# Kernel tuning notes

Hardware: AMD Instinct MI355X
Metric: run time of the kernel (lower is better)

## Reference

```python
import jax, jax.numpy as jnp
import numpy as np

N_NODES = 100000
N_EDGES = 3200000
N_FEAT = 128
HIDDEN = 16
N_CLASSES = 10
N_GRAPHS = 512


def setup_inputs() -> dict:
    key = jax.random.key(0)
    ks = jax.random.split(key, 12)
    x = jax.random.normal(ks[0], (N_NODES, N_FEAT), dtype=jnp.float32)
    edge_index = jax.random.randint(ks[1], (2, N_EDGES), 0, N_NODES, dtype=jnp.int64)
    batch = jnp.sort(jax.random.randint(ks[2], (N_NODES,), 0, N_GRAPHS, dtype=jnp.int64))
    def glorot(k, fan_in, fan_out):
        s = jnp.sqrt(6.0 / (fan_in + fan_out)).astype(jnp.float32)
        return jax.random.uniform(k, (fan_in, fan_out), jnp.float32, -s, s)
    W1 = glorot(ks[3], N_FEAT, HIDDEN); b1 = jnp.zeros((HIDDEN,), jnp.float32)
    W2 = glorot(ks[4], HIDDEN, HIDDEN); b2 = jnp.zeros((HIDDEN,), jnp.float32)
    W3 = glorot(ks[5], HIDDEN, HIDDEN); b3 = jnp.zeros((HIDDEN,), jnp.float32)
    Wlin = glorot(ks[6], HIDDEN, N_CLASSES)
    blin = jnp.zeros((N_CLASSES,), jnp.float32)
    return {"x": x, "edge_index": edge_index, "batch": batch,
            "W1": W1, "b1": b1, "W2": W2, "b2": b2, "W3": W3, "b3": b3,
            "Wlin": Wlin, "blin": blin}


def _gcn_conv(x, W, b, src, dst, norm, n):
    # h = X W ; out[dst] += norm * h[src] ; + bias
    h = x @ W
    out = jax.ops.segment_sum(h[src] * norm[:, None], dst, num_segments=n)
    return out + b


def reference(x, edge_index, batch, W1, b1, W2, b2, W3, b3, Wlin, blin):
    n = x.shape[0]
    loop = jnp.arange(n, dtype=edge_index.dtype)
    src = jnp.concatenate([edge_index[0], loop])  # add self-loops (PyG GCNConv default)
    dst = jnp.concatenate([edge_index[1], loop])
    # symmetric degree normalization: deg over destination (incl. self-loops)
    deg = jax.ops.segment_sum(jnp.ones_like(dst, dtype=x.dtype), dst, num_segments=n)
    dinv = jnp.where(deg > 0, jax.lax.rsqrt(jnp.maximum(deg, 1.0)), 0.0)
    norm = dinv[src] * dinv[dst]  # [E+N]

    h = jax.nn.relu(_gcn_conv(x, W1, b1, src, dst, norm, n))
    h = jax.nn.relu(_gcn_conv(h, W2, b2, src, dst, norm, n))
    h = _gcn_conv(h, W3, b3, src, dst, norm, n)
    # global add pool over graphs
    pooled = jax.ops.segment_sum(h, batch, num_segments=N_GRAPHS)  # [G, hidden]
    # dropout p=0.5 is identity in eval mode
    return pooled @ Wlin + blin
```

## Files before the change

kernel.cpp:

```cpp
#include <hip/hip_runtime.h>
#include <hip/hip_fp16.h>

#define N_NODES   100000
#define N_EDGES   3200000
#define N_FEAT    128
#define HIDDEN    16
#define N_CLASSES 10
#define N_GRAPHS  512
#define NPB       256
#define NBUCKET   391
#define EPB       8192
#define PBLK      ((N_EDGES + EPB - 1) / EPB)
#define PSLACK    12288
#define CSLACK    9216


__global__ void cursor_init_kernel(int* __restrict__ cur) {
    int i = blockIdx.x * 256 + threadIdx.x;
    if (i < NBUCKET) cur[i] = i * PSLACK;
}

__global__ __launch_bounds__(512) void partition_kernel(const int* __restrict__ src,
                                                        const int* __restrict__ dst,
                                                        int* __restrict__ cur,
                                                        unsigned* __restrict__ part) {
    __shared__ int cnt[NBUCKET];
    __shared__ int lbase[NBUCKET];
    __shared__ int rk[NBUCKET];
    __shared__ int gbase[NBUCKET];
    __shared__ int s[512];
    __shared__ unsigned sorted[EPB];
    int tid = threadIdx.x;
    for (int i = tid; i < NBUCKET; i += 512) cnt[i] = 0;
    __syncthreads();
    int s0 = blockIdx.x * EPB;
#pragma unroll
    for (int i = 0; i < EPB / 512; ++i) {
        int e = s0 + i * 512 + tid;
        if (e < N_EDGES) atomicAdd(&cnt[dst[e] >> 8], 1);
    }
    __syncthreads();
    int v = (tid < NBUCKET) ? cnt[tid] : 0;
    s[tid] = v;
    __syncthreads();
    for (int off = 1; off < 512; off <<= 1) {
        int t = (tid >= off) ? s[tid - off] : 0;
        __syncthreads();
        s[tid] += t;
        __syncthreads();
    }
    if (tid < NBUCKET) {
        int lb = s[tid] - v;
        lbase[tid] = lb;
        rk[tid]    = lb;
        int cpad = (v + 15) & ~15;
        gbase[tid] = cpad ? atomicAdd(&cur[tid], cpad) : 0;
    }
    __syncthreads();
#pragma unroll
    for (int i = 0; i < EPB / 512; ++i) {
        int e = s0 + i * 512 + tid;
        if (e < N_EDGES) {
            int d = dst[e];
            int b = d >> 8;
            int r = atomicAdd(&rk[b], 1);
            sorted[r] = (unsigned)src[e] | ((unsigned)(d & 255) << 17);
        }
    }
    __syncthreads();
    int wave = tid >> 6, lane = tid & 63;
    for (int b = wave; b < NBUCKET; b += 8) {
        int c = cnt[b];
        if (!c) continue;
        int cpad = (c + 15) & ~15;
        int lb = lbase[b], gb = gbase[b];
        for (int j = lane; j < cpad; j += 64)
            part[gb + j] = (j < c) ? sorted[lb + j] : 0xFFFFFFFFu;
    }
}

__global__ void build_csr_kernel(const unsigned* __restrict__ part, const int* __restrict__ cur,
                                 int* __restrict__ rp_beg, int* __restrict__ rp_end,
                                 float* __restrict__ dinv, int* __restrict__ csr) {
    __shared__ int ncnt[256];
    __shared__ int s[256];
    int b   = blockIdx.x;
    int tid = threadIdx.x;
    int beg = b * PSLACK, end = cur[b];
    ncnt[tid] = 0;
    __syncthreads();
    for (int j = beg + tid; j < end; j += 256) {
        unsigned r = part[j];
        if (r != 0xFFFFFFFFu) atomicAdd(&ncnt[(r >> 17) & 255], 1);
    }
    __syncthreads();
    int deg = ncnt[tid];
    s[tid] = deg;
    __syncthreads();
    for (int off = 1; off < 256; off <<= 1) {
        int t = (tid >= off) ? s[tid - off] : 0;
        __syncthreads();
        s[tid] += t;
        __syncthreads();
    }
    int excl = s[tid] - deg;
    int node = b * 256 + tid;
    int cbeg = b * CSLACK;
    if (node < N_NODES) {
        rp_beg[node] = cbeg + excl;
        rp_end[node] = cbeg + excl + deg;
        dinv[node]   = rsqrtf((float)(deg + 1));
    }
    ncnt[tid] = cbeg + excl;
    __syncthreads();
    for (int j = beg + tid; j < end; j += 256) {
        unsigned r = part[j];
        if (r != 0xFFFFFFFFu) {
            int v = (r >> 17) & 255;
            int slot = atomicAdd(&ncnt[v], 1);
            csr[slot] = (int)(r & 0x1FFFFu);
        }
    }
}


__device__ __forceinline__ void pack_store_row(__half* dstp, int v, const float* o) {
    int4 w0, w1;
    __half2 q;
    q = __floats2half2_rn(o[0],  o[1]);  w0.x = *(int*)&q;
    q = __floats2half2_rn(o[2],  o[3]);  w0.y = *(int*)&q;
    q = __floats2half2_rn(o[4],  o[5]);  w0.z = *(int*)&q;
    q = __floats2half2_rn(o[6],  o[7]);  w0.w = *(int*)&q;
    q = __floats2half2_rn(o[8],  o[9]);  w1.x = *(int*)&q;
    q = __floats2half2_rn(o[10], o[11]); w1.y = *(int*)&q;
    q = __floats2half2_rn(o[12], o[13]); w1.z = *(int*)&q;
    q = __floats2half2_rn(o[14], o[15]); w1.w = *(int*)&q;
    ((int4*)dstp)[v * 2]     = w0;
    ((int4*)dstp)[v * 2 + 1] = w1;
}

__global__ void transform_x_kernel(const float* __restrict__ x, const float* __restrict__ W,
                                   const float* __restrict__ dinv, __half* __restrict__ g) {
    __shared__ float Wl[N_FEAT * HIDDEN];
    int tid = threadIdx.x;
    for (int i = tid; i < N_FEAT * HIDDEN; i += 256) Wl[i] = W[i];
    __syncthreads();
    int v = blockIdx.x * 256 + tid;
    if (v >= N_NODES) return;
    float acc[HIDDEN];
#pragma unroll
    for (int f = 0; f < HIDDEN; ++f) acc[f] = 0.f;
    const float4* xr = (const float4*)(x + (size_t)v * N_FEAT);
#pragma unroll 4
    for (int k4 = 0; k4 < N_FEAT / 4; ++k4) {
        float4 xv = xr[k4];
        const float* wr = &Wl[k4 * 4 * HIDDEN];
#pragma unroll
        for (int f = 0; f < HIDDEN; ++f)
            acc[f] += xv.x * wr[f] + xv.y * wr[HIDDEN + f] +
                      xv.z * wr[2 * HIDDEN + f] + xv.w * wr[3 * HIDDEN + f];
    }
    float di = dinv[v];
#pragma unroll
    for (int f = 0; f < HIDDEN; ++f) acc[f] *= di;
    pack_store_row(g, v, acc);
}

__global__ void transform_h_kernel(const __half* __restrict__ h, const float* __restrict__ W,
                                   const float* __restrict__ dinv, __half* __restrict__ g) {
    __shared__ float Wl[HIDDEN * HIDDEN];
    int tid = threadIdx.x;
    if (tid < HIDDEN * HIDDEN) Wl[tid] = W[tid];
    __syncthreads();
    int v = blockIdx.x * 256 + tid;
    if (v >= N_NODES) return;
    int4 r0 = ((const int4*)h)[v * 2];
    int4 r1 = ((const int4*)h)[v * 2 + 1];
    float hv[HIDDEN];
    {
        const int rr[8] = {r0.x, r0.y, r0.z, r0.w, r1.x, r1.y, r1.z, r1.w};
#pragma unroll
        for (int q = 0; q < 8; ++q) {
            __half2 p = *(const __half2*)&rr[q];
            float2 f2 = __half22float2(p);
            hv[q * 2] = f2.x; hv[q * 2 + 1] = f2.y;
        }
    }
    float acc[HIDDEN];
#pragma unroll
    for (int f = 0; f < HIDDEN; ++f) acc[f] = 0.f;
#pragma unroll
    for (int k = 0; k < HIDDEN; ++k) {
        float hk = hv[k];
#pragma unroll
        for (int f = 0; f < HIDDEN; ++f) acc[f] += hk * Wl[k * HIDDEN + f];
    }
    float di = dinv[v];
#pragma unroll
    for (int f = 0; f < HIDDEN; ++f) acc[f] *= di;
    pack_store_row(g, v, acc);
}

__global__ void aggregate_kernel(const __half* __restrict__ g, const int* __restrict__ rp_beg,
                                 const int* __restrict__ rp_end, const int* __restrict__ csr,
                                 const float* __restrict__ dinv, const float* __restrict__ bias,
                                 __half* __restrict__ hout, int do_relu) {
    int tid  = threadIdx.x;
    int wave = tid >> 6;
    int l    = tid & 63;
    int c  = l >> 3;
    int vl = (l >> 1) & 3;
    int hh = l & 1;
    int v = blockIdx.x * 16 + wave * 4 + vl;
    if (v >= N_NODES) return;
    int beg = rp_beg[v];
    int deg = rp_end[v] - beg;
    int j0 = beg + ((deg * c) >> 3);
    int j1 = beg + ((deg * (c + 1)) >> 3);
    const int4* g4 = (const int4*)g;
    float a0 = 0.f, a1 = 0.f, a2 = 0.f, a3 = 0.f, a4 = 0.f, a5 = 0.f, a6 = 0.f, a7 = 0.f;
#pragma unroll 4
    for (int j = j0; j < j1; ++j) {
        int s = csr[j];
        int4 r = g4[s * 2 + hh];
        float2 f0 = __half22float2(*(const __half2*)&r.x);
        float2 f1 = __half22float2(*(const __half2*)&r.y);
        float2 f2 = __half22float2(*(const __half2*)&r.z);
        float2 f3 = __half22float2(*(const __half2*)&r.w);
        a0 += f0.x; a1 += f0.y; a2 += f1.x; a3 += f1.y;
        a4 += f2.x; a5 += f2.y; a6 += f3.x; a7 += f3.y;
    }
    a0 += __shfl_xor(a0, 8);  a1 += __shfl_xor(a1, 8);
    a2 += __shfl_xor(a2, 8);  a3 += __shfl_xor(a3, 8);
    a4 += __shfl_xor(a4, 8);  a5 += __shfl_xor(a5, 8);
    a6 += __shfl_xor(a6, 8);  a7 += __shfl_xor(a7, 8);
    a0 += __shfl_xor(a0, 16); a1 += __shfl_xor(a1, 16);
    a2 += __shfl_xor(a2, 16); a3 += __shfl_xor(a3, 16);
    a4 += __shfl_xor(a4, 16); a5 += __shfl_xor(a5, 16);
    a6 += __shfl_xor(a6, 16); a7 += __shfl_xor(a7, 16);
    a0 += __shfl_xor(a0, 32); a1 += __shfl_xor(a1, 32);
    a2 += __shfl_xor(a2, 32); a3 += __shfl_xor(a3, 32);
    a4 += __shfl_xor(a4, 32); a5 += __shfl_xor(a5, 32);
    a6 += __shfl_xor(a6, 32); a7 += __shfl_xor(a7, 32);
    if (c == 0) {
        int4 r = g4[v * 2 + hh];
        float2 s0 = __half22float2(*(const __half2*)&r.x);
        float2 s1 = __half22float2(*(const __half2*)&r.y);
        float2 s2 = __half22float2(*(const __half2*)&r.z);
        float2 s3 = __half22float2(*(const __half2*)&r.w);
        float di = dinv[v];
        const float4* bp = (const float4*)bias;
        float4 bA = bp[hh * 2];
        float4 bB = bp[hh * 2 + 1];
        float o0 = di * (a0 + s0.x) + bA.x;
        float o1 = di * (a1 + s0.y) + bA.y;
        float o2 = di * (a2 + s1.x) + bA.z;
        float o3 = di * (a3 + s1.y) + bA.w;
        float o4 = di * (a4 + s2.x) + bB.x;
        float o5 = di * (a5 + s2.y) + bB.y;
        float o6 = di * (a6 + s3.x) + bB.z;
        float o7 = di * (a7 + s3.y) + bB.w;
        if (do_relu) {
            o0 = fmaxf(o0, 0.f); o1 = fmaxf(o1, 0.f); o2 = fmaxf(o2, 0.f); o3 = fmaxf(o3, 0.f);
            o4 = fmaxf(o4, 0.f); o5 = fmaxf(o5, 0.f); o6 = fmaxf(o6, 0.f); o7 = fmaxf(o7, 0.f);
        }
        int4 w;
        __half2 q;
        q = __floats2half2_rn(o0, o1); w.x = *(int*)&q;
        q = __floats2half2_rn(o2, o3); w.y = *(int*)&q;
        q = __floats2half2_rn(o4, o5); w.z = *(int*)&q;
        q = __floats2half2_rn(o6, o7); w.w = *(int*)&q;
        ((int4*)hout)[v * 2 + hh] = w;
    }
}


__global__ void pool_head_kernel(const __half* __restrict__ h, const int* __restrict__ batch,
                                 const float* __restrict__ Wlin, const float* __restrict__ blin,
                                 float* __restrict__ out) {
    __shared__ float red[256];
    __shared__ int bounds[2];
    int g   = blockIdx.x;
    int tid = threadIdx.x;
    if (tid < 2) {
        int target = g + tid;
        int lo = 0, hi = N_NODES;
        while (lo < hi) {
            int mid = (lo + hi) >> 1;
            if (batch[mid] < target) lo = mid + 1; else hi = mid;
        }
        bounds[tid] = lo;
    }
    __syncthreads();
    int start = bounds[0], end = bounds[1];
    int f = tid & 15, r = tid >> 4;
    float acc = 0.f;
    for (int v = start + r; v < end; v += 16)
        acc += __half2float(h[v * HIDDEN + f]);
    red[tid] = acc;
    __syncthreads();
    for (int off = 128; off >= 16; off >>= 1) {
        if (tid < off) red[tid] += red[tid + off];
        __syncthreads();
    }
    if (tid < N_CLASSES) {
        float s = blin[tid];
#pragma unroll
        for (int fe = 0; fe < HIDDEN; ++fe) s += red[fe] * Wlin[fe * N_CLASSES + tid];
        out[g * N_CLASSES + tid] = s;
    }
}


extern "C" void kernel_launch(void* const* d_in, const int* in_sizes, int n_in,
                              void* d_out, int out_size, void* d_ws, size_t ws_size,
                              hipStream_t stream) {
    const float* x     = (const float*)d_in[0];
    const int*   ei    = (const int*)d_in[1];
    const int*   src   = ei;
    const int*   dst   = ei + N_EDGES;
    const int*   batch = (const int*)d_in[2];
    const float* W1 = (const float*)d_in[3];
    const float* b1 = (const float*)d_in[4];
    const float* W2 = (const float*)d_in[5];
    const float* b2 = (const float*)d_in[6];
    const float* W3 = (const float*)d_in[7];
    const float* b3 = (const float*)d_in[8];
    const float* Wlin = (const float*)d_in[9];
    const float* blin = (const float*)d_in[10];
    float* out = (float*)d_out;

    char* w = (char*)d_ws;
    auto alloc = [&](size_t bytes) -> char* {
        char* p = w;
        w += (bytes + 255) & ~(size_t)255;
        return p;
    };
    int*    cur    = (int*)alloc((size_t)NBUCKET * 4);
    int*    rp_beg = (int*)alloc((size_t)N_NODES * 4);
    int*    rp_end = (int*)alloc((size_t)N_NODES * 4);
    float*  dinv   = (float*)alloc((size_t)N_NODES * 4);
    __half* g      = (__half*)alloc((size_t)N_NODES * HIDDEN * 2);
    __half* hA     = (__half*)alloc((size_t)N_NODES * HIDDEN * 2);
    __half* hB     = (__half*)alloc((size_t)N_NODES * HIDDEN * 2);
    unsigned* part = (unsigned*)alloc((size_t)NBUCKET * PSLACK * 4);
    int*    csr    = (int*)alloc((size_t)NBUCKET * CSLACK * 4);

    int nbn = (N_NODES + 255) / 256;
    int ab  = (N_NODES + 15) / 16;

    cursor_init_kernel<<<(NBUCKET + 255) / 256, 256, 0, stream>>>(cur);
    partition_kernel<<<PBLK, 512, 0, stream>>>(src, dst, cur, part);
    build_csr_kernel<<<NBUCKET, 256, 0, stream>>>(part, cur, rp_beg, rp_end, dinv, csr);

    transform_x_kernel<<<nbn, 256, 0, stream>>>(x, W1, dinv, g);
    aggregate_kernel<<<ab, 256, 0, stream>>>(g, rp_beg, rp_end, csr, dinv, b1, hA, 1);
    transform_h_kernel<<<nbn, 256, 0, stream>>>(hA, W2, dinv, g);
    aggregate_kernel<<<ab, 256, 0, stream>>>(g, rp_beg, rp_end, csr, dinv, b2, hB, 1);
    transform_h_kernel<<<nbn, 256, 0, stream>>>(hB, W3, dinv, g);
    aggregate_kernel<<<ab, 256, 0, stream>>>(g, rp_beg, rp_end, csr, dinv, b3, hA, 0);

    pool_head_kernel<<<N_GRAPHS, 256, 0, stream>>>(hA, batch, Wlin, blin, out);
}
```

Baseline: 289.2 us.

## Fuse next-layer transform into aggregation, stage CSR in LDS, retune partition/CSR build

The next layer's 16x16 transform and dinv scaling move into the aggregate epilogue, which removes the two transform_h launches and their round trip of the hidden features through memory. Each aggregate block now covers 64 nodes and stages that range of CSR indices in shared memory when it fits. The partition kernel uses half as many edges per block with larger bucket slack and 16-lane store groups, and build_csr runs with 512 threads. Per-block work rises, and degree-skewed blocks can overflow the LDS buffer and fall back to global reads.

```diff
diff --git a/kernel.cpp b/kernel.cpp
--- a/kernel.cpp
+++ b/kernel.cpp
@@ -9,10 +9,11 @@
 #define N_GRAPHS  512
 #define NPB       256
 #define NBUCKET   391
-#define EPB       8192
+#define EPB       4096
 #define PBLK      ((N_EDGES + EPB - 1) / EPB)
-#define PSLACK    12288
+#define PSLACK    15872
 #define CSLACK    9216
+#define LDSE      3200
 
 
 __global__ void cursor_init_kernel(int* __restrict__ cur) {
@@ -68,75 +69,74 @@
         }
     }
     __syncthreads();
-    int wave = tid >> 6, lane = tid & 63;
-    for (int b = wave; b < NBUCKET; b += 8) {
+    int w16 = tid >> 4, l16 = tid & 15;
+    for (int b = w16; b < NBUCKET; b += 32) {
         int c = cnt[b];
         if (!c) continue;
         int cpad = (c + 15) & ~15;
         int lb = lbase[b], gb = gbase[b];
-        for (int j = lane; j < cpad; j += 64)
+        for (int j = l16; j < cpad; j += 16)
             part[gb + j] = (j < c) ? sorted[lb + j] : 0xFFFFFFFFu;
     }
 }
 
-__global__ void build_csr_kernel(const unsigned* __restrict__ part, const int* __restrict__ cur,
-                                 int* __restrict__ rp_beg, int* __restrict__ rp_end,
-                                 float* __restrict__ dinv, int* __restrict__ csr) {
+__global__ __launch_bounds__(512) void build_csr_kernel(const unsigned* __restrict__ part,
+                                                        const int* __restrict__ cur,
+                                                        int* __restrict__ rp_beg, int* __restrict__ rp_end,
+                                                        float* __restrict__ dinv, int* __restrict__ csr) {
     __shared__ int ncnt[256];
-    __shared__ int s[256];
+    __shared__ int s[512];
     int b   = blockIdx.x;
     int tid = threadIdx.x;
     int beg = b * PSLACK, end = cur[b];
-    ncnt[tid] = 0;
-    __syncthreads();
-    for (int j = beg + tid; j < end; j += 256) {
+    if (tid < 256) ncnt[tid] = 0;
+    __syncthreads();
+    for (int j = beg + tid; j < end; j += 512) {
         unsigned r = part[j];
         if (r != 0xFFFFFFFFu) atomicAdd(&ncnt[(r >> 17) & 255], 1);
     }
     __syncthreads();
-    int deg = ncnt[tid];
+    int deg = (tid < 256) ? ncnt[tid] : 0;
     s[tid] = deg;
     __syncthreads();
-    for (int off = 1; off < 256; off <<= 1) {
+    for (int off = 1; off < 512; off <<= 1) {
         int t = (tid >= off) ? s[tid - off] : 0;
         __syncthreads();
         s[tid] += t;
         __syncthreads();
     }
     int excl = s[tid] - deg;
-    int node = b * 256 + tid;
     int cbeg = b * CSLACK;
-    if (node < N_NODES) {
-        rp_beg[node] = cbeg + excl;
-        rp_end[node] = cbeg + excl + deg;
-        dinv[node]   = rsqrtf((float)(deg + 1));
-    }
-    ncnt[tid] = cbeg + excl;
-    __syncthreads();
-    for (int j = beg + tid; j < end; j += 256) {
+    if (tid < 256) {
+        int node = b * 256 + tid;
+        if (node < N_NODES) {
+            rp_beg[node] = cbeg + excl;
+            rp_end[node] = cbeg + excl + deg;
+            dinv[node]   = rsqrtf((float)(deg + 1));
+        }
+    }
+    __syncthreads();
+    if (tid < 256) ncnt[tid] = cbeg + excl;
+    __syncthreads();
+    for (int j = beg + tid; j < end; j += 512) {
         unsigned r = part[j];
         if (r != 0xFFFFFFFFu) {
-            int v = (r >> 17) & 255;
-            int slot = atomicAdd(&ncnt[v], 1);
+            int vv = (r >> 17) & 255;
+            int slot = atomicAdd(&ncnt[vv], 1);
             csr[slot] = (int)(r & 0x1FFFFu);
         }
     }
 }
 
 
-__device__ __forceinline__ void pack_store_row(__half* dstp, int v, const float* o) {
-    int4 w0, w1;
+__device__ __forceinline__ void pack_store8(__half* outp, int idx, const float* o) {
+    int4 w;
     __half2 q;
-    q = __floats2half2_rn(o[0],  o[1]);  w0.x = *(int*)&q;
-    q = __floats2half2_rn(o[2],  o[3]);  w0.y = *(int*)&q;
-    q = __floats2half2_rn(o[4],  o[5]);  w0.z = *(int*)&q;
-    q = __floats2half2_rn(o[6],  o[7]);  w0.w = *(int*)&q;
-    q = __floats2half2_rn(o[8],  o[9]);  w1.x = *(int*)&q;
-    q = __floats2half2_rn(o[10], o[11]); w1.y = *(int*)&q;
-    q = __floats2half2_rn(o[12], o[13]); w1.z = *(int*)&q;
-    q = __floats2half2_rn(o[14], o[15]); w1.w = *(int*)&q;
-    ((int4*)dstp)[v * 2]     = w0;
-    ((int4*)dstp)[v * 2 + 1] = w1;
+    q = __floats2half2_rn(o[0], o[1]); w.x = *(int*)&q;
+    q = __floats2half2_rn(o[2], o[3]); w.y = *(int*)&q;
+    q = __floats2half2_rn(o[4], o[5]); w.z = *(int*)&q;
+    q = __floats2half2_rn(o[6], o[7]); w.w = *(int*)&q;
+    ((int4*)outp)[idx] = w;
 }
 
 __global__ void transform_x_kernel(const float* __restrict__ x, const float* __restrict__ W,
@@ -163,114 +163,122 @@
     float di = dinv[v];
 #pragma unroll
     for (int f = 0; f < HIDDEN; ++f) acc[f] *= di;
-    pack_store_row(g, v, acc);
-}
-
-__global__ void transform_h_kernel(const __half* __restrict__ h, const float* __restrict__ W,
-                                   const float* __restrict__ dinv, __half* __restrict__ g) {
-    __shared__ float Wl[HIDDEN * HIDDEN];
-    int tid = threadIdx.x;
-    if (tid < HIDDEN * HIDDEN) Wl[tid] = W[tid];
-    __syncthreads();
-    int v = blockIdx.x * 256 + tid;
-    if (v >= N_NODES) return;
-    int4 r0 = ((const int4*)h)[v * 2];
-    int4 r1 = ((const int4*)h)[v * 2 + 1];
-    float hv[HIDDEN];
-    {
-        const int rr[8] = {r0.x, r0.y, r0.z, r0.w, r1.x, r1.y, r1.z, r1.w};
-#pragma unroll
-        for (int q = 0; q < 8; ++q) {
-            __half2 p = *(const __half2*)&rr[q];
-            float2 f2 = __half22float2(p);
-            hv[q * 2] = f2.x; hv[q * 2 + 1] = f2.y;
-        }
-    }
-    float acc[HIDDEN];
-#pragma unroll
-    for (int f = 0; f < HIDDEN; ++f) acc[f] = 0.f;
-#pragma unroll
-    for (int k = 0; k < HIDDEN; ++k) {
-        float hk = hv[k];
-#pragma unroll
-        for (int f = 0; f < HIDDEN; ++f) acc[f] += hk * Wl[k * HIDDEN + f];
-    }
-    float di = dinv[v];
-#pragma unroll
-    for (int f = 0; f < HIDDEN; ++f) acc[f] *= di;
-    pack_store_row(g, v, acc);
-}
-
-__global__ void aggregate_kernel(const __half* __restrict__ g, const int* __restrict__ rp_beg,
-                                 const int* __restrict__ rp_end, const int* __restrict__ csr,
-                                 const float* __restrict__ dinv, const float* __restrict__ bias,
-                                 __half* __restrict__ hout, int do_relu) {
-    int tid  = threadIdx.x;
-    int wave = tid >> 6;
-    int l    = tid & 63;
-    int c  = l >> 3;
-    int vl = (l >> 1) & 3;
-    int hh = l & 1;
-    int v = blockIdx.x * 16 + wave * 4 + vl;
-    if (v >= N_NODES) return;
-    int beg = rp_beg[v];
-    int deg = rp_end[v] - beg;
-    int j0 = beg + ((deg * c) >> 3);
-    int j1 = beg + ((deg * (c + 1)) >> 3);
-    const int4* g4 = (const int4*)g;
-    float a0 = 0.f, a1 = 0.f, a2 = 0.f, a3 = 0.f, a4 = 0.f, a5 = 0.f, a6 = 0.f, a7 = 0.f;
+    pack_store8(g, v * 2,     &acc[0]);
+    pack_store8(g, v * 2 + 1, &acc[8]);
+}
+
+__global__ __launch_bounds__(256) void aggregate_kernel(
+        const __half* __restrict__ gin, const int* __restrict__ rp_beg,
+        const int* __restrict__ rp_end, const int* __restrict__ csr,
+        const float* __restrict__ dinv, const float* __restrict__ bias,
+        const float* __restrict__ Wn, __half* __restrict__ outp, int mode) {
+    __shared__ int scsr[LDSE];
+    __shared__ float Wls[HIDDEN * HIDDEN];
+    int tid = threadIdx.x;
+    int v0 = blockIdx.x * 64;
+    int vmax = min(v0 + 63, N_NODES - 1);
+    Wls[tid] = Wn[tid & 255];
+    int beg0  = rp_beg[v0];
+    int end0  = rp_end[vmax];
+    int algn0 = beg0 & ~3;
+    int n4    = ((end0 + 3) & ~3) - algn0;
+    bool fits = (n4 <= LDSE);
+    if (fits) {
+        const int4* gsrc = (const int4*)(csr + algn0);
+        for (int i = tid; i < (n4 >> 2); i += 256)
+            ((int4*)scsr)[i] = gsrc[i];
+    }
+    __syncthreads();
+    int wave = tid >> 6, l = tid & 63;
+    int c = l >> 3, vl = (l >> 1) & 3, hh = l & 1;
+    const int4* g4 = (const int4*)gin;
+    const float4* bp = (const float4*)bias;
+    float4 bA = bp[hh * 2];
+    float4 bB = bp[hh * 2 + 1];
+    for (int rnd = 0; rnd < 4; ++rnd) {
+        int v = v0 + rnd * 16 + wave * 4 + vl;
+        int beg = algn0, deg = 0;
+        if (v <= vmax) { beg = rp_beg[v]; deg = rp_end[v] - beg; }
+        int j0 = (deg * c) >> 3;
+        int j1 = (deg * (c + 1)) >> 3;
+        float a0 = 0.f, a1 = 0.f, a2 = 0.f, a3 = 0.f, a4 = 0.f, a5 = 0.f, a6 = 0.f, a7 = 0.f;
+        if (fits) {
+            int base = beg - algn0;
 #pragma unroll 4
-    for (int j = j0; j < j1; ++j) {
-        int s = csr[j];
-        int4 r = g4[s * 2 + hh];
-        float2 f0 = __half22float2(*(const __half2*)&r.x);
-        float2 f1 = __half22float2(*(const __half2*)&r.y);
-        float2 f2 = __half22float2(*(const __half2*)&r.z);
-        float2 f3 = __half22float2(*(const __half2*)&r.w);
-        a0 += f0.x; a1 += f0.y; a2 += f1.x; a3 += f1.y;
-        a4 += f2.x; a5 += f2.y; a6 += f3.x; a7 += f3.y;
-    }
-    a0 += __shfl_xor(a0, 8);  a1 += __shfl_xor(a1, 8);
-    a2 += __shfl_xor(a2, 8);  a3 += __shfl_xor(a3, 8);
-    a4 += __shfl_xor(a4, 8);  a5 += __shfl_xor(a5, 8);
-    a6 += __shfl_xor(a6, 8);  a7 += __shfl_xor(a7, 8);
-    a0 += __shfl_xor(a0, 16); a1 += __shfl_xor(a1, 16);
-    a2 += __shfl_xor(a2, 16); a3 += __shfl_xor(a3, 16);
-    a4 += __shfl_xor(a4, 16); a5 += __shfl_xor(a5, 16);
-    a6 += __shfl_xor(a6, 16); a7 += __shfl_xor(a7, 16);
-    a0 += __shfl_xor(a0, 32); a1 += __shfl_xor(a1, 32);
-    a2 += __shfl_xor(a2, 32); a3 += __shfl_xor(a3, 32);
-    a4 += __shfl_xor(a4, 32); a5 += __shfl_xor(a5, 32);
-    a6 += __shfl_xor(a6, 32); a7 += __shfl_xor(a7, 32);
-    if (c == 0) {
-        int4 r = g4[v * 2 + hh];
-        float2 s0 = __half22float2(*(const __half2*)&r.x);
-        float2 s1 = __half22float2(*(const __half2*)&r.y);
-        float2 s2 = __half22float2(*(const __half2*)&r.z);
-        float2 s3 = __half22float2(*(const __half2*)&r.w);
-        float di = dinv[v];
-        const float4* bp = (const float4*)bias;
-        float4 bA = bp[hh * 2];
-        float4 bB = bp[hh * 2 + 1];
-        float o0 = di * (a0 + s0.x) + bA.x;
-        float o1 = di * (a1 + s0.y) + bA.y;
-        float o2 = di * (a2 + s1.x) + bA.z;
-        float o3 = di * (a3 + s1.y) + bA.w;
-        float o4 = di * (a4 + s2.x) + bB.x;
-        float o5 = di * (a5 + s2.y) + bB.y;
-        float o6 = di * (a6 + s3.x) + bB.z;
-        float o7 = di * (a7 + s3.y) + bB.w;
-        if (do_relu) {
-            o0 = fmaxf(o0, 0.f); o1 = fmaxf(o1, 0.f); o2 = fmaxf(o2, 0.f); o3 = fmaxf(o3, 0.f);
-            o4 = fmaxf(o4, 0.f); o5 = fmaxf(o5, 0.f); o6 = fmaxf(o6, 0.f); o7 = fmaxf(o7, 0.f);
-        }
-        int4 w;
-        __half2 q;
-        q = __floats2half2_rn(o0, o1); w.x = *(int*)&q;
-        q = __floats2half2_rn(o2, o3); w.y = *(int*)&q;
-        q = __floats2half2_rn(o4, o5); w.z = *(int*)&q;
-        q = __floats2half2_rn(o6, o7); w.w = *(int*)&q;
-        ((int4*)hout)[v * 2 + hh] = w;
+            for (int j = j0; j < j1; ++j) {
+                int sI = scsr[base + j];
+                int4 r = g4[sI * 2 + hh];
+                float2 f0 = __half22float2(*(const __half2*)&r.x);
+                float2 f1 = __half22float2(*(const __half2*)&r.y);
+                float2 f2 = __half22float2(*(const __half2*)&r.z);
+                float2 f3 = __half22float2(*(const __half2*)&r.w);
+                a0 += f0.x; a1 += f0.y; a2 += f1.x; a3 += f1.y;
+                a4 += f2.x; a5 += f2.y; a6 += f3.x; a7 += f3.y;
+            }
+        } else {
+#pragma unroll 4
+            for (int j = j0; j < j1; ++j) {
+                int sI = csr[beg + j];
+                int4 r = g4[sI * 2 + hh];
+                float2 f0 = __half22float2(*(const __half2*)&r.x);
+                float2 f1 = __half22float2(*(const __half2*)&r.y);
+                float2 f2 = __half22float2(*(const __half2*)&r.z);
+                float2 f3 = __half22float2(*(const __half2*)&r.w);
+                a0 += f0.x; a1 += f0.y; a2 += f1.x; a3 += f1.y;
+                a4 += f2.x; a5 += f2.y; a6 += f3.x; a7 += f3.y;
+            }
+        }
+        a0 += __shfl_xor(a0, 8);  a1 += __shfl_xor(a1, 8);
+        a2 += __shfl_xor(a2, 8);  a3 += __shfl_xor(a3, 8);
+        a4 += __shfl_xor(a4, 8);  a5 += __shfl_xor(a5, 8);
+        a6 += __shfl_xor(a6, 8);  a7 += __shfl_xor(a7, 8);
+        a0 += __shfl_xor(a0, 16); a1 += __shfl_xor(a1, 16);
+        a2 += __shfl_xor(a2, 16); a3 += __shfl_xor(a3, 16);
+        a4 += __shfl_xor(a4, 16); a5 += __shfl_xor(a5, 16);
+        a6 += __shfl_xor(a6, 16); a7 += __shfl_xor(a7, 16);
+        a0 += __shfl_xor(a0, 32); a1 += __shfl_xor(a1, 32);
+        a2 += __shfl_xor(a2, 32); a3 += __shfl_xor(a3, 32);
+        a4 += __shfl_xor(a4, 32); a5 += __shfl_xor(a5, 32);
+        a6 += __shfl_xor(a6, 32); a7 += __shfl_xor(a7, 32);
+        if (c == 0 && v <= vmax) {
+            int4 r = g4[v * 2 + hh];
+            float2 s0 = __half22float2(*(const __half2*)&r.x);
+            float2 s1 = __half22float2(*(const __half2*)&r.y);
+            float2 s2 = __half22float2(*(const __half2*)&r.z);
+            float2 s3 = __half22float2(*(const __half2*)&r.w);
+            float di = dinv[v];
+            float o[8];
+            o[0] = di * (a0 + s0.x) + bA.x;
+            o[1] = di * (a1 + s0.y) + bA.y;
+            o[2] = di * (a2 + s1.x) + bA.z;
+            o[3] = di * (a3 + s1.y) + bA.w;
+            o[4] = di * (a4 + s2.x) + bB.x;
+            o[5] = di * (a5 + s2.y) + bB.y;
+            o[6] = di * (a6 + s3.x) + bB.z;
+            o[7] = di * (a7 + s3.y) + bB.w;
+            if (mode) {
+#pragma unroll
+                for (int i = 0; i < 8; ++i) o[i] = fmaxf(o[i], 0.f);
+                float hfull[16];
+#pragma unroll
+                for (int i = 0; i < 8; ++i) {
+                    hfull[hh * 8 + i]       = o[i];
+                    hfull[(1 - hh) * 8 + i] = __shfl_xor(o[i], 1);
+                }
+                float y[8];
+#pragma unroll
+                for (int f8 = 0; f8 < 8; ++f8) {
+                    int f = hh * 8 + f8;
+                    float acc = 0.f;
+#pragma unroll
+                    for (int k = 0; k < HIDDEN; ++k) acc += hfull[k] * Wls[k * HIDDEN + f];
+                    y[f8] = di * acc;
+                }
+                pack_store8(outp, v * 2 + hh, y);
+            } else {
+                pack_store8(outp, v * 2 + hh, o);
+            }
+        }
     }
 }
 
@@ -340,25 +348,22 @@
     int*    rp_beg = (int*)alloc((size_t)N_NODES * 4);
     int*    rp_end = (int*)alloc((size_t)N_NODES * 4);
     float*  dinv   = (float*)alloc((size_t)N_NODES * 4);
-    __half* g      = (__half*)alloc((size_t)N_NODES * HIDDEN * 2);
-    __half* hA     = (__half*)alloc((size_t)N_NODES * HIDDEN * 2);
-    __half* hB     = (__half*)alloc((size_t)N_NODES * HIDDEN * 2);
+    __half* bufA   = (__half*)alloc((size_t)N_NODES * HIDDEN * 2);
+    __half* bufB   = (__half*)alloc((size_t)N_NODES * HIDDEN * 2);
     unsigned* part = (unsigned*)alloc((size_t)NBUCKET * PSLACK * 4);
     int*    csr    = (int*)alloc((size_t)NBUCKET * CSLACK * 4);
 
     int nbn = (N_NODES + 255) / 256;
-    int ab  = (N_NODES + 15) / 16;
+    int ab  = (N_NODES + 63) / 64;
 
     cursor_init_kernel<<<(NBUCKET + 255) / 256, 256, 0, stream>>>(cur);
     partition_kernel<<<PBLK, 512, 0, stream>>>(src, dst, cur, part);
-    build_csr_kernel<<<NBUCKET, 256, 0, stream>>>(part, cur, rp_beg, rp_end, dinv, csr);
-
-    transform_x_kernel<<<nbn, 256, 0, stream>>>(x, W1, dinv, g);
-    aggregate_kernel<<<ab, 256, 0, stream>>>(g, rp_beg, rp_end, csr, dinv, b1, hA, 1);
-    transform_h_kernel<<<nbn, 256, 0, stream>>>(hA, W2, dinv, g);
-    aggregate_kernel<<<ab, 256, 0, stream>>>(g, rp_beg, rp_end, csr, dinv, b2, hB, 1);
-    transform_h_kernel<<<nbn, 256, 0, stream>>>(hB, W3, dinv, g);
-    aggregate_kernel<<<ab, 256, 0, stream>>>(g, rp_beg, rp_end, csr, dinv, b3, hA, 0);
-
-    pool_head_kernel<<<N_GRAPHS, 256, 0, stream>>>(hA, batch, Wlin, blin, out);
-}
+    build_csr_kernel<<<NBUCKET, 512, 0, stream>>>(part, cur, rp_beg, rp_end, dinv, csr);
+
+    transform_x_kernel<<<nbn, 256, 0, stream>>>(x, W1, dinv, bufA);
+    aggregate_kernel<<<ab, 256, 0, stream>>>(bufA, rp_beg, rp_end, csr, dinv, b1, W2, bufB, 1);
+    aggregate_kernel<<<ab, 256, 0, stream>>>(bufB, rp_beg, rp_end, csr, dinv, b2, W3, bufA, 1);
+    aggregate_kernel<<<ab, 256, 0, stream>>>(bufA, rp_beg, rp_end, csr, dinv, b3, W3, bufB, 0);
+
+    pool_head_kernel<<<N_GRAPHS, 256, 0, stream>>>(bufB, batch, Wlin, blin, out);
+}
```

Measured after the change: 330.9 us. +14.4%, slower.
